# Performance work log

Hardware: AMD Instinct MI355X
Metric: run time of the kernel (lower is better)

The kernel has to match this reference:

```python
import jax, jax.numpy as jnp
import numpy as np
from jax.scipy.special import gammaln

# NQ_IN + 4 == 2*H is required because the two kernel=1, padding=1 convs grow the
# length axis by 4 and the following nn.Linear(2H, H) acts on the length axis.
B, NQ_IN, NK, QDIM, KDIM, H = 16, 2044, 1024, 80, 256, 1024


def setup_inputs() -> dict:
    ks = jax.random.split(jax.random.key(0), 14)
    s = 0.02
    return {
        "query": jax.random.normal(ks[0], (B, NQ_IN, QDIM), jnp.float32),
        "key": jax.random.normal(ks[1], (B, NK, KDIM), jnp.float32),
        "query_lens": jnp.full((B,), 2 * H, jnp.int32),
        "key_lens": jnp.full((B,), NK, jnp.int32),
        # query branch params (Conv1d k=1 stored as (out,in); Linear as (out,in))
        "qc1_w": jax.random.normal(ks[2], (2 * H, QDIM), jnp.float32) * s,
        "qc1_b": jax.random.normal(ks[3], (2 * H,), jnp.float32) * s,
        "qc2_w": jax.random.normal(ks[4], (2 * H, 2 * H), jnp.float32) * s,
        "qc2_b": jax.random.normal(ks[5], (2 * H,), jnp.float32) * s,
        "ql_w": jax.random.normal(ks[6], (H, 2 * H), jnp.float32) * s,
        "ql_b": jax.random.normal(ks[7], (H,), jnp.float32) * s,
        # key branch params
        "kc_w": jax.random.normal(ks[8], (H, KDIM, 3), jnp.float32) * s,
        "kc_b": jax.random.normal(ks[9], (H,), jnp.float32) * s,
        "kl1_w": jax.random.normal(ks[10], (2 * H, H), jnp.float32) * s,
        "kl1_b": jax.random.normal(ks[11], (2 * H,), jnp.float32) * s,
        "kl2_w": jax.random.normal(ks[12], (H, 2 * H), jnp.float32) * s,
        "kl2_b": jax.random.normal(ks[13], (H,), jnp.float32) * s,
    }


def _log_beta_binom(query_lens, key_lens, tq, tk):
    # Standard MAS beta-binomial alignment prior over a (tq, tk) grid.
    i = jnp.arange(tq, dtype=jnp.float32)[None, :, None]
    j = jnp.arange(tk, dtype=jnp.float32)[None, None, :]
    ql = query_lens.astype(jnp.float32)[:, None, None]
    kl = key_lens.astype(jnp.float32)[:, None, None]
    a = i + 1.0
    b = jnp.maximum(ql - i, 1.0)
    n = jnp.maximum(kl - 1.0, 0.0)
    nmj = jnp.maximum(n - j, 0.0)

    def betaln(x, y):
        return gammaln(x) + gammaln(y) - gammaln(x + y)

    logp = (gammaln(n + 1.0) - gammaln(j + 1.0) - gammaln(nmj + 1.0)
            + betaln(j + a, nmj + b) - betaln(a, b))
    valid = (i < ql) & (j < kl)
    return jnp.where(valid, logp, -1e9)


def _forward(query, key, query_lens, key_lens,
             qc1_w, qc1_b, qc2_w, qc2_b, ql_w, ql_b,
             kc_w, kc_b, kl1_w, kl1_b, kl2_w, kl2_b):
    # query branch: b n c -> b c n, two k=1/p=1 convs (pad length, pointwise), Linear over LENGTH axis
    q = jnp.transpose(query, (0, 2, 1))                       # (B, QDIM, NQ_IN)
    q = jnp.pad(q, ((0, 0), (0, 0), (1, 1)))
    q = jnp.einsum('bcn,oc->bon', q, qc1_w) + qc1_b[None, :, None]   # (B, 2H, NQ_IN+2)
    q = jnp.pad(q, ((0, 0), (0, 0), (1, 1)))
    q = jnp.einsum('bcn,oc->bon', q, qc2_w) + qc2_b[None, :, None]   # (B, 2H, 2H)
    q = jnp.einsum('bcn,hn->bch', q, ql_w) + ql_b                    # (B, 2H, H) Linear on length axis

    # key branch: b n c -> b c n, Conv1d k=3 p=1, then two Linears over LENGTH axis
    k = jnp.transpose(key, (0, 2, 1))                         # (B, KDIM, NK)
    k = jax.lax.conv_general_dilated(k, kc_w, (1,), ((1, 1),),
                                     dimension_numbers=('NCH', 'OIH', 'NCH'))
    k = k + kc_b[None, :, None]                               # (B, H, NK=H)
    k = jnp.einsum('bcn,on->bco', k, kl1_w) + kl1_b           # (B, H, 2H)
    k = jnp.einsum('bco,ho->bch', k, kl2_w) + kl2_b           # (B, H, H)

    # dist = -cdist(q, k), computed via the GEMM form (same as torch.cdist mm mode)
    sq = (jnp.sum(q * q, -1)[:, :, None] + jnp.sum(k * k, -1)[:, None, :]
          - 2.0 * jnp.einsum('bnd,bmd->bnm', q, k))           # (B, 2H, H)
    dist = -jnp.sqrt(jnp.maximum(sq, 1e-12))

    prior = _log_beta_binom(query_lens, key_lens, q.shape[1], k.shape[1])
    return jax.nn.log_softmax(dist + prior, axis=-1)


def reference(query, key, query_lens, key_lens,
              qc1_w, qc1_b, qc2_w, qc2_b, ql_w, ql_b,
              kc_w, kc_b, kl1_w, kl1_b, kl2_w, kl2_b):
    return _forward(query, key, query_lens, key_lens,
                    qc1_w, qc1_b, qc2_w, qc2_b, ql_w, ql_b,
                    kc_w, kc_b, kl1_w, kl1_b, kl2_w, kl2_b)
```

## Files before the change

### kernel.cpp

```cpp
#include <hip/hip_runtime.h>
#include <math.h>

typedef unsigned short u16;
typedef float floatx4 __attribute__((ext_vector_type(4)));
typedef __bf16 bf16x8 __attribute__((ext_vector_type(8)));

#define BB   16
#define TQ   2048
#define TK   1024
#define HH   1024
#define H2   2048
#define QD   80
#define QDP  128
#define KD   256
#define NQ   2044
#define NKEY 1024
#define T12N 3072

__device__ __forceinline__ u16 f2bf(float f) {
  unsigned int u = __float_as_uint(f);
  u = u + 0x7fffu + ((u >> 16) & 1u);
  return (u16)(u >> 16);
}
__device__ __forceinline__ float bf2f(u16 s) {
  return __uint_as_float(((unsigned int)s) << 16);
}
__device__ __forceinline__ float tgf(const float* __restrict__ tbl, int x) {
  return tbl[(x < 8191) ? (x < 0 ? 0 : x) : 8191];
}

__global__ __launch_bounds__(256) void prep_all_k(
    const float* __restrict__ qc2_w, const float* __restrict__ kl2_w,
    const float* __restrict__ ql_w, const float* __restrict__ kc_w,
    const float* __restrict__ kl1_w,
    u16* __restrict__ qc2w, u16* __restrict__ kl2w, u16* __restrict__ qlw2,
    u16* __restrict__ kcp, float* __restrict__ colsum1, float* __restrict__ tbl)
{
  long b = blockIdx.x;
  const int t = threadIdx.x;
  __shared__ float red[256];
  if (b < 16384) {
    long i = b * 256 + t; qc2w[i] = f2bf(qc2_w[i]); return;
  }
  b -= 16384;
  if (b < 8192) {
    long i = b * 256 + t; kl2w[i] = f2bf(kl2_w[i]); return;
  }
  b -= 8192;
  if (b < 8192) {
    long i = b * 256 + t;
    int n = (int)(i & 2047);
    int h = (int)(i >> 11);
    qlw2[i] = (n < NQ) ? f2bf(ql_w[(long)h * H2 + n + 2]) : (u16)0; return;
  }
  b -= 8192;
  if (b < 3072) {
    long i = b * 256 + t;
    int r = (int)(i % 768);
    int o = (int)(i / 768);
    int tt = r >> 8, d = r & 255;
    kcp[i] = f2bf(kc_w[((long)o * KD + d) * 3 + tt]); return;
  }
  b -= 3072;
  if (b < 2048) {
    const float* row = kl1_w + b * (long)HH;
    float s = row[t] + row[t + 256] + row[t + 512] + row[t + 768];
    red[t] = s; __syncthreads();
    for (int st = 128; st > 0; st >>= 1) { if (t < st) red[t] += red[t + st]; __syncthreads(); }
    if (!t) colsum1[b] = red[0];
    return;
  }
  b -= 2048;
  { int i = (int)(b * 256 + t); if (i < 8192) tbl[i] = i ? (float)lgamma((double)i) : 0.0f; }
}

__global__ __launch_bounds__(256) void tpack_k(
    const float* __restrict__ kl1_w, const float* __restrict__ qc1_w,
    const float* __restrict__ query,
    u16* __restrict__ kl1T, u16* __restrict__ qc1T, u16* __restrict__ qT)
{
  __shared__ float tile[64][65];
  int bid = blockIdx.x;
  const int tid = threadIdx.x;
  const int r4 = tid >> 6, c = tid & 63;
  const float* src; u16* dst;
  int sr0, sc0, srcR, srcC, srcStride, dstC;
  if (bid < 512) {
    sr0 = (bid >> 4) * 64; sc0 = (bid & 15) * 64;
    src = kl1_w; srcR = 2048; srcC = 1024; srcStride = 1024;
    dst = kl1T; dstC = 2048;
  } else if ((bid -= 512) < 64) {
    sr0 = (bid >> 1) * 64; sc0 = (bid & 1) * 64;
    src = qc1_w; srcR = 2048; srcC = QD; srcStride = QD;
    dst = qc1T; dstC = 2048;
  } else {
    bid -= 64;
    const int b16 = bid >> 6, r = bid & 63;
    sr0 = (r >> 1) * 64; sc0 = (r & 1) * 64;
    src = query + (long)b16 * NQ * QD; srcR = NQ; srcC = QD; srcStride = QD;
    dst = qT + (long)b16 * QDP * 2048; dstC = 2048;
  }
#pragma unroll
  for (int rr = r4; rr < 64; rr += 4) {
    const int gr = sr0 + rr, gc = sc0 + c;
    tile[rr][c] = (gr < srcR && gc < srcC) ? src[(long)gr * srcStride + gc] : 0.f;
  }
  __syncthreads();
#pragma unroll
  for (int rr = r4; rr < 64; rr += 4)
    dst[(long)(sc0 + rr) * dstC + sr0 + c] = f2bf(tile[c][rr]);
}

__global__ __launch_bounds__(256) void pack_kcolT_k(const float* __restrict__ key, u16* __restrict__ out) {
  __shared__ float tile[64][65];
  const int bid = blockIdx.x, tid = threadIdx.x;
  const int b = bid >> 6, r = bid & 63;
  const int m0 = (r >> 2) * 64;
  const int d0 = (r & 3) * 64;
  const int r4 = tid >> 6, c = tid & 63;
#pragma unroll
  for (int rr = r4; rr < 64; rr += 4)
    tile[rr][c] = key[((long)b * NKEY + m0 + rr) * KD + d0 + c];
  __syncthreads();
#pragma unroll
  for (int t = 0; t < 3; t++) {
    const int n = m0 + 1 - t + c;
    if (n >= 0 && n < NKEY) {
#pragma unroll
      for (int rr = r4; rr < 64; rr += 4)
        out[((long)b * 768 + t * 256 + d0 + rr) * NKEY + n] = f2bf(tile[c][rr]);
    }
  }
  if (m0 == 0 && c == 0) {
#pragma unroll
    for (int rr = r4; rr < 64; rr += 4)
      out[((long)b * 768 + d0 + rr) * NKEY + 0] = (u16)0;
  }
  if (m0 == 960 && c == 0) {
#pragma unroll
    for (int rr = r4; rr < 64; rr += 4)
      out[((long)b * 768 + 512 + d0 + rr) * NKEY + (NKEY - 1)] = (u16)0;
  }
}

__global__ __launch_bounds__(256) void fold_bias_k(
    const float* __restrict__ qc2_w, const float* __restrict__ qc1_b, const float* __restrict__ qc2_b,
    const float* __restrict__ kl2_w, const float* __restrict__ kl1_b, const float* __restrict__ kl2_b,
    const float* __restrict__ ql_w, const float* __restrict__ colsum1,
    float* __restrict__ bqm, float* __restrict__ bkv, float* __restrict__ s1v, float* __restrict__ s0v,
    float* __restrict__ wsum)
{
  const int bid = blockIdx.x, t = threadIdx.x;
  float s = 0.f, s2 = 0.f;
  if (bid < H2) {
    const float* row = qc2_w + (long)bid * H2;
    for (int k = t; k < H2; k += 256) s += row[k] * qc1_b[k];
  } else if (bid < H2 + HH) {
    const float* row = kl2_w + (long)(bid - H2) * H2;
    for (int k = t; k < H2; k += 256) { const float rv = row[k]; s += rv * kl1_b[k]; s2 += rv * colsum1[k]; }
  } else {
    const float* row = ql_w + (long)(bid - H2 - HH) * H2;
    for (int m = 1 + t; m <= H2 - 2; m += 256) s += row[m];
  }
  __shared__ float red[256];
  __shared__ float red2[256];
  red[t] = s; red2[t] = s2; __syncthreads();
  for (int st = 128; st > 0; st >>= 1) {
    if (t < st) { red[t] += red[t + st]; red2[t] += red2[t + st]; }
    __syncthreads();
  }
  if (!t) {
    if (bid < H2) bqm[bid] = red[0] + qc2_b[bid];
    else if (bid < H2 + HH) { bkv[bid - H2] = red[0] + kl2_b[bid - H2]; wsum[bid - H2] = red2[0]; }
    else {
      int h = bid - H2 - HH;
      s1v[h] = red[0];
      s0v[h] = ql_w[(long)h * H2] + ql_w[(long)h * H2 + H2 - 1];
    }
  }
}

__device__ __forceinline__ void gld_lds16(const u16* g, u16* l) {
  __builtin_amdgcn_global_load_lds((const __attribute__((address_space(1))) void*)g,
                                   (__attribute__((address_space(3))) void*)l, 16, 0, 0);
}

template<int OUTF32>
__global__ __launch_bounds__(256) void gemm_bt(
    const u16* __restrict__ A, const u16* __restrict__ B, void* __restrict__ Cv,
    int M, int N, int K, int lda, int ldb, int swap, int kspl,
    long sA, long sB, long sC, long sN,
    const float* __restrict__ colb, const float* __restrict__ rowb,
    const float* __restrict__ r1m, const float* __restrict__ r1n,
    const float* __restrict__ r2m, const float* __restrict__ r2n)
{
  __shared__ __align__(16) u16 As[128 * 32];
  __shared__ __align__(16) u16 Bs[128 * 32];
  const int bz = blockIdx.z;
  const int bb_ = (kspl > 1) ? bz / kspl : bz;
  const int ks_ = (kspl > 1) ? bz - bb_ * kspl : 0;
  const int tid  = threadIdx.x;
  const int lane = tid & 63;
  const int wv = tid >> 6;
  const int wm = ((tid >> 7) & 1) * 64;
  const int wn = ((tid >> 6) & 1) * 64;
  const int m0 = (swap ? blockIdx.x : blockIdx.y) * 128;
  const int n0 = (swap ? blockIdx.y : blockIdx.x) * 128;

  const int srow = wv * 32 + (lane >> 2);
  const int scol = (lane & 3) << 3;
  const u16* ga = A + bb_ * sA + (long)ks_ * K + (long)(m0 + srow) * lda + scol;
  const u16* gb = B + bb_ * sB + (long)ks_ * K + (long)(n0 + srow) * ldb + scol;
  u16* la0 = &As[(wv * 32) * 32];
  u16* la1 = &As[(wv * 32 + 16) * 32];
  u16* lb0 = &Bs[(wv * 32) * 32];
  u16* lb1 = &Bs[(wv * 32 + 16) * 32];
  const long a16 = (long)16 * lda;
  const long b16 = (long)16 * ldb;

  floatx4 acc[4][4];
#pragma unroll
  for (int a_ = 0; a_ < 4; a_++)
#pragma unroll
    for (int b_ = 0; b_ < 4; b_++) acc[a_][b_] = (floatx4){0.f, 0.f, 0.f, 0.f};

  const int fr = lane & 15;
  const int fk = (lane >> 4) << 3;

  for (int kb = 0; kb < K; kb += 32) {
    gld_lds16(ga,       la0);
    gld_lds16(ga + a16, la1);
    gld_lds16(gb,       lb0);
    gld_lds16(gb + b16, lb1);
    ga += 32; gb += 32;
    __syncthreads();
    bf16x8 af[4], bfr[4];
#pragma unroll
    for (int mi = 0; mi < 4; mi++)
      af[mi] = *reinterpret_cast<const bf16x8*>(&As[(wm + mi * 16 + fr) * 32 + fk]);
#pragma unroll
    for (int ni = 0; ni < 4; ni++)
      bfr[ni] = *reinterpret_cast<const bf16x8*>(&Bs[(wn + ni * 16 + fr) * 32 + fk]);
#pragma unroll
    for (int mi = 0; mi < 4; mi++)
#pragma unroll
      for (int ni = 0; ni < 4; ni++)
        acc[mi][ni] = __builtin_amdgcn_mfma_f32_16x16x32_bf16(af[mi], bfr[ni], acc[mi][ni], 0, 0, 0);
    __syncthreads();
  }

  const int fr4 = (lane >> 4) << 2;
  const int fc  = lane & 15;
  u16*   Cb16 = (u16*)Cv + (long)bz * sC;
  float* Cb32 = (float*)Cv + (long)bz * sC;
  const float* cbp  = colb ? colb + (long)bb_ * sN : nullptr;
  const float* r1np = r1n ? r1n + (long)bb_ * sN : nullptr;
  const float* r2np = r2n ? r2n + (long)bb_ * sN : nullptr;
#pragma unroll
  for (int mi = 0; mi < 4; mi++) {
#pragma unroll
    for (int ni = 0; ni < 4; ni++) {
      const int gm0 = m0 + wm + mi * 16 + fr4;
      const int gn  = n0 + wn + ni * 16 + fc;
      const float cbv  = cbp ? cbp[gn] : 0.f;
      const float r1nv = r1np ? r1np[gn] : 0.f;
      const float r2nv = r2np ? r2np[gn] : 0.f;
#pragma unroll
      for (int rr = 0; rr < 4; rr++) {
        const int gm = gm0 + rr;
        float v = acc[mi][ni][rr] + cbv;
        if (rowb) v += rowb[gm];
        if (r1m)  v += r1m[gm] * r1nv;
        if (r2m)  v += r2m[gm] * r2nv;
        if (OUTF32) Cb32[(long)gm * N + gn] = v;
        else        Cb16[(long)gm * N + gn] = f2bf(v);
      }
    }
  }
}

__global__ __launch_bounds__(256) void reduce_bk_k(const float* __restrict__ P, u16* __restrict__ out,
                                                   long chunk, int S, long total) {
  long j = ((long)blockIdx.x * 256 + threadIdx.x) * 4;
  if (j >= total) return;
  long b = j / chunk;
  const float* p = P + j + b * chunk * (S - 1);
  float4 s = *reinterpret_cast<const float4*>(p);
  for (int t = 1; t < S; t++) {
    const float4 v = *reinterpret_cast<const float4*>(p + (long)t * chunk);
    s.x += v.x; s.y += v.y; s.z += v.z; s.w += v.w;
  }
  union { u16 h[4]; uint2 u; } o;
  o.h[0] = f2bf(s.x); o.h[1] = f2bf(s.y); o.h[2] = f2bf(s.z); o.h[3] = f2bf(s.w);
  *reinterpret_cast<uint2*>(out + j) = o.u;
}

__global__ __launch_bounds__(256) void u_k(
    const u16* __restrict__ TpT, const float* __restrict__ qlb,
    const float* __restrict__ s1, const float* __restrict__ s0,
    const float* __restrict__ tbl, const int* __restrict__ qlens, const int* __restrict__ klens,
    float* __restrict__ u0, float* __restrict__ u1, float* __restrict__ u2,
    float* __restrict__ sc, float* __restrict__ c1,
    float* __restrict__ crow, float* __restrict__ t12)
{
  const int bid = blockIdx.x, t = threadIdx.x;
  __shared__ float4 red[256];
  if (bid < BB * QDP) {
    uint2 v = reinterpret_cast<const uint2*>(TpT + (long)bid * HH)[t];
    float a0 = bf2f((u16)(v.x & 0xffff)), a1 = bf2f((u16)(v.x >> 16));
    float a2 = bf2f((u16)(v.y & 0xffff)), a3 = bf2f((u16)(v.y >> 16));
    float4 q  = reinterpret_cast<const float4*>(qlb)[t];
    float4 w1 = reinterpret_cast<const float4*>(s1)[t];
    float4 w0 = reinterpret_cast<const float4*>(s0)[t];
    float4 s;
    s.x = a0 * q.x  + a1 * q.y  + a2 * q.z  + a3 * q.w;
    s.y = a0 * w1.x + a1 * w1.y + a2 * w1.z + a3 * w1.w;
    s.z = a0 * w0.x + a1 * w0.y + a2 * w0.z + a3 * w0.w;
    s.w = 0.f;
    red[t] = s; __syncthreads();
    for (int st = 128; st > 0; st >>= 1) {
      if (t < st) { red[t].x += red[t + st].x; red[t].y += red[t + st].y; red[t].z += red[t + st].z; }
      __syncthreads();
    }
    if (!t) { u0[bid] = red[0].x; u1[bid] = red[0].y; u2[bid] = red[0].z; }
  } else if (bid < BB * QDP + 6) {
    const int idx = bid - BB * QDP;
    const float* X = (idx == 1 || idx == 5) ? s1 : (idx == 2) ? s0 : qlb;
    const float* Y = (idx == 1 || idx == 3) ? s1 : (idx == 0) ? qlb : s0;
    float4 x = reinterpret_cast<const float4*>(X)[t];
    float4 y = reinterpret_cast<const float4*>(Y)[t];
    float4 s; s.x = x.x * y.x + x.y * y.y + x.z * y.z + x.w * y.w; s.y = s.z = s.w = 0.f;
    red[t] = s; __syncthreads();
    for (int st = 128; st > 0; st >>= 1) {
      if (t < st) red[t].x += red[t + st].x;
      __syncthreads();
    }
    if (!t) sc[idx] = red[0].x;
  } else if (bid < BB * QDP + 6 + 64) {
    const int idx = bid - (BB * QDP + 6);
    const int b = idx >> 2;
    const int j = ((idx & 3) << 8) | t;
    const int kl = klens[b];
    const int n_ = (kl - 1 > 0) ? kl - 1 : 0;
    c1[b * TK + j] = tgf(tbl, j + 1) + tgf(tbl, n_ - j + 1);
  } else if (bid < BB * QDP + 6 + 64 + 128) {
    const int idx = bid - (BB * QDP + 6 + 64);
    const int b = idx >> 3;
    const int i = ((idx & 7) << 8) | t;
    const int ql = qlens[b], kl = klens[b];
    const int n_ = (kl - 1 > 0) ? kl - 1 : 0;
    const int bb = (ql - i > 1) ? ql - i : 1;
    crow[b * TQ + i] = tgf(tbl, n_ + 1) + tgf(tbl, i + 1 + bb) - tgf(tbl, i + 1)
                     - tgf(tbl, bb) - tgf(tbl, i + 1 + n_ + bb);
  } else {
    const int idx = bid - (BB * QDP + 6 + 64 + 128);
    const int b = idx / 12;
    const int s = (idx - b * 12) * 256 + t;
    const int ql = qlens[b], kl = klens[b];
    const int n_ = (kl - 1 > 0) ? kl - 1 : 0;
    t12[b * T12N + s] = tgf(tbl, s + 1) + tgf(tbl, n_ + ql - s);
  }
}

__global__ __launch_bounds__(256) void qn_k(
    const u16* __restrict__ Wq, const float* __restrict__ WqG,
    const float* __restrict__ u0, const float* __restrict__ u1, const float* __restrict__ u2,
    const float* __restrict__ bqm, const float* __restrict__ qc2_b,
    const float* __restrict__ sc, float* __restrict__ qn)
{
  const int bx = blockIdx.x, t = threadIdx.x;
  const int b = bx >> 10;
  const int i = ((bx & 1023) << 1) | (t >> 7);
  const int d = t & 127;
  const float w  = bf2f(Wq[(long)i * QDP + d]);
  const float g  = WqG[((long)b * H2 + i) * QDP + d];
  const float bq = bqm[i], q2 = qc2_b[i];
  const float uu = u0[b * QDP + d] + bq * u1[b * QDP + d] + q2 * u2[b * QDP + d];
  __shared__ float red[256];
  red[t] = w * (g + 2.f * uu); __syncthreads();
  for (int s = 64; s > 0; s >>= 1) { if ((t & 127) < s) red[t] += red[t + s]; __syncthreads(); }
  if (d == 0) {
    const float cst = sc[0] + bq * bq * sc[1] + q2 * q2 * sc[2]
                    + 2.f * (bq * sc[3] + q2 * sc[4] + bq * q2 * sc[5]);
    qn[b * TQ + i] = red[t] + cst;
  }
}

__global__ __launch_bounds__(256) void rownormk_k(
    const u16* __restrict__ K3, const float* __restrict__ qlb,
    const float* __restrict__ s1, const float* __restrict__ s0,
    float* __restrict__ kn, float* __restrict__ yb, float* __restrict__ y1, float* __restrict__ y0)
{
  const long r = blockIdx.x;
  const int t = threadIdx.x;
  uint2 v = reinterpret_cast<const uint2*>(K3 + r * HH)[t];
  float a0 = bf2f((u16)(v.x & 0xffff)), a1 = bf2f((u16)(v.x >> 16));
  float a2 = bf2f((u16)(v.y & 0xffff)), a3 = bf2f((u16)(v.y >> 16));
  float4 q  = reinterpret_cast<const float4*>(qlb)[t];
  float4 w1 = reinterpret_cast<const float4*>(s1)[t];
  float4 w0 = reinterpret_cast<const float4*>(s0)[t];
  float4 s;
  s.x = a0 * a0   + a1 * a1   + a2 * a2   + a3 * a3;
  s.y = a0 * q.x  + a1 * q.y  + a2 * q.z  + a3 * q.w;
  s.z = a0 * w1.x + a1 * w1.y + a2 * w1.z + a3 * w1.w;
  s.w = a0 * w0.x + a1 * w0.y + a2 * w0.z + a3 * w0.w;
  __shared__ float4 red[256];
  red[t] = s; __syncthreads();
  for (int st = 128; st > 0; st >>= 1) {
    if (t < st) {
      red[t].x += red[t + st].x; red[t].y += red[t + st].y;
      red[t].z += red[t + st].z; red[t].w += red[t + st].w;
    }
    __syncthreads();
  }
  if (!t) { kn[r] = red[0].x; yb[r] = red[0].y; y1[r] = red[0].z; y0[r] = red[0].w; }
}

#define L2E 1.4426950408889634f
__global__ __launch_bounds__(1024) void smax_k(
    const u16* __restrict__ Wq, const u16* __restrict__ Z2, float* __restrict__ out,
    const float* __restrict__ ybv, const float* __restrict__ y1v, const float* __restrict__ y0v,
    const float* __restrict__ bqmv, const float* __restrict__ qc2_b,
    const float* __restrict__ qnv, const float* __restrict__ knv, const float* __restrict__ c1v,
    const float* __restrict__ crowv, const float* __restrict__ t12v,
    const int* __restrict__ qlens, const int* __restrict__ klens)
{
  __shared__ __align__(16) float wst[16][32 * 36];
  __shared__ float t12s[1152];
  __shared__ float jA[1024], jB[1024], jC[1024], jc1[1024];
  __shared__ float qns[128], crs[128], bqms[128], q2bs[128];
  __shared__ float lseb[4][128];
  __shared__ float lsef[128];

  const int b = blockIdx.x, mt = blockIdx.y;
  const int m0 = mt * 128;
  const int t = threadIdx.x;
  const int w = t >> 6, lane = t & 63;
  const int wm2 = (w >> 2) * 32;
  const int wn2 = (w & 3) * 32;
  const int fr = lane & 15, fk = (lane >> 4) << 3;
  const int fr4 = (lane >> 4) << 2, fc = lane & 15;
  const int qlv = qlens[b], klv = klens[b];

  if (t < 128) {
    qns[t]  = qnv[(long)b * TQ + m0 + t];
    crs[t]  = crowv[(long)b * TQ + m0 + t];
    bqms[t] = bqmv[m0 + t];
    q2bs[t] = qc2_b[m0 + t];
  }
  for (int k = t; k < 1152; k += 1024) t12s[k] = t12v[(long)b * T12N + m0 + k];
  {
    const int j = t;
    const float kn = knv[(long)b * TK + j];
    const float yb = ybv[(long)b * TK + j];
    const float y1 = y1v[(long)b * TK + j];
    const float y0 = y0v[(long)b * TK + j];
    jA[j]  = kn - 2.f * yb;
    jB[j]  = -2.f * y1;
    jC[j]  = -2.f * y0;
    jc1[j] = c1v[(long)b * TK + j];
  }

  bf16x8 af[4][2];
#pragma unroll
  for (int kc = 0; kc < 4; kc++)
#pragma unroll
    for (int mi = 0; mi < 2; mi++)
      af[kc][mi] = *reinterpret_cast<const bf16x8*>(
          Wq + (long)(m0 + wm2 + mi * 16 + fr) * QDP + kc * 32 + fk);

  const u16* Zb = Z2 + (long)b * TK * QDP;
  float* outp = out + (long)b * TQ * TK + (long)m0 * TK;

  float s_[8];
#pragma unroll
  for (int ri = 0; ri < 8; ri++) s_[ri] = 0.f;

  __syncthreads();

  for (int nt = 0; nt < 8; nt++) {
    bf16x8 bfr[4][2];
#pragma unroll
    for (int kc = 0; kc < 4; kc++)
#pragma unroll
      for (int nj = 0; nj < 2; nj++)
        bfr[kc][nj] = *reinterpret_cast<const bf16x8*>(
            Zb + (long)(nt * 128 + wn2 + nj * 16 + fr) * QDP + kc * 32 + fk);

    floatx4 acc[2][2];
#pragma unroll
    for (int mi = 0; mi < 2; mi++)
#pragma unroll
      for (int nj = 0; nj < 2; nj++) acc[mi][nj] = (floatx4){0.f, 0.f, 0.f, 0.f};
#pragma unroll
    for (int kc = 0; kc < 4; kc++)
#pragma unroll
      for (int mi = 0; mi < 2; mi++)
#pragma unroll
        for (int nj = 0; nj < 2; nj++)
          acc[mi][nj] = __builtin_amdgcn_mfma_f32_16x16x32_bf16(af[kc][mi], bfr[kc][nj], acc[mi][nj], 0, 0, 0);

    int gj[2]; float Aj[2], Bj[2], Cj[2], Dj[2];
#pragma unroll
    for (int nj = 0; nj < 2; nj++) {
      gj[nj] = nt * 128 + wn2 + nj * 16 + fc;
      Aj[nj] = jA[gj[nj]]; Bj[nj] = jB[gj[nj]]; Cj[nj] = jC[gj[nj]]; Dj[nj] = jc1[gj[nj]];
    }

#pragma unroll
    for (int mi = 0; mi < 2; mi++) {
#pragma unroll
      for (int rr = 0; rr < 4; rr++) {
        const int rl = wm2 + mi * 16 + fr4 + rr;
        const float qnr = qns[rl], crr = crs[rl], bqr = bqms[rl], q2r = q2bs[rl];
        const bool rowok = (m0 + rl) < qlv;
        const int ri = mi * 4 + rr;
#pragma unroll
        for (int nj = 0; nj < 2; nj++) {
          const float sq = fmaxf(qnr + Aj[nj] + bqr * Bj[nj] + q2r * Cj[nj]
                                 - 2.0f * acc[mi][nj][rr], 1e-12f);
          const float x = -__builtin_amdgcn_sqrtf(sq) + crr - Dj[nj] + t12s[rl + gj[nj]];
          const float vv = (rowok && gj[nj] < klv) ? x : -1e9f;
          s_[ri] += exp2f(vv * L2E);
        }
      }
    }
  }

#pragma unroll
  for (int k2 = 1; k2 <= 8; k2 <<= 1) {
#pragma unroll
    for (int ri = 0; ri < 8; ri++) s_[ri] += __shfl_xor(s_[ri], k2, 64);
  }
  if (fc == 0) {
#pragma unroll
    for (int mi = 0; mi < 2; mi++)
#pragma unroll
      for (int rr = 0; rr < 4; rr++)
        lseb[w & 3][wm2 + mi * 16 + fr4 + rr] = s_[mi * 4 + rr];
  }
  __syncthreads();
  if (t < 128) {
    const float tot = (lseb[0][t] + lseb[1][t]) + (lseb[2][t] + lseb[3][t]);
    lsef[t] = (tot > 0.f) ? logf(tot) : (-1e9f + logf((float)TK));
  }
  __syncthreads();

  float lse_r[8];
#pragma unroll
  for (int mi = 0; mi < 2; mi++)
#pragma unroll
    for (int rr = 0; rr < 4; rr++)
      lse_r[mi * 4 + rr] = lsef[wm2 + mi * 16 + fr4 + rr];

  float* wstw = wst[w];
  for (int nt = 0; nt < 8; nt++) {
    bf16x8 bfr[4][2];
#pragma unroll
    for (int kc = 0; kc < 4; kc++)
#pragma unroll
      for (int nj = 0; nj < 2; nj++)
        bfr[kc][nj] = *reinterpret_cast<const bf16x8*>(
            Zb + (long)(nt * 128 + wn2 + nj * 16 + fr) * QDP + kc * 32 + fk);

    floatx4 acc[2][2];
#pragma unroll
    for (int mi = 0; mi < 2; mi++)
#pragma unroll
      for (int nj = 0; nj < 2; nj++) acc[mi][nj] = (floatx4){0.f, 0.f, 0.f, 0.f};
#pragma unroll
    for (int kc = 0; kc < 4; kc++)
#pragma unroll
      for (int mi = 0; mi < 2; mi++)
#pragma unroll
        for (int nj = 0; nj < 2; nj++)
          acc[mi][nj] = __builtin_amdgcn_mfma_f32_16x16x32_bf16(af[kc][mi], bfr[kc][nj], acc[mi][nj], 0, 0, 0);

    int gj[2]; float Aj[2], Bj[2], Cj[2], Dj[2];
#pragma unroll
    for (int nj = 0; nj < 2; nj++) {
      gj[nj] = nt * 128 + wn2 + nj * 16 + fc;
      Aj[nj] = jA[gj[nj]]; Bj[nj] = jB[gj[nj]]; Cj[nj] = jC[gj[nj]]; Dj[nj] = jc1[gj[nj]];
    }

#pragma unroll
    for (int mi = 0; mi < 2; mi++) {
#pragma unroll
      for (int rr = 0; rr < 4; rr++) {
        const int rl = wm2 + mi * 16 + fr4 + rr;
        const float qnr = qns[rl], crr = crs[rl], bqr = bqms[rl], q2r = q2bs[rl];
        const bool rowok = (m0 + rl) < qlv;
        const float l = lse_r[mi * 4 + rr];
#pragma unroll
        for (int nj = 0; nj < 2; nj++) {
          const float sq = fmaxf(qnr + Aj[nj] + bqr * Bj[nj] + q2r * Cj[nj]
                                 - 2.0f * acc[mi][nj][rr], 1e-12f);
          const float x = -__builtin_amdgcn_sqrtf(sq) + crr - Dj[nj] + t12s[rl + gj[nj]];
          const float vv = (rowok && gj[nj] < klv) ? x : -1e9f;
          wstw[(mi * 16 + fr4 + rr) * 36 + nj * 16 + fc] = vv - l;
        }
      }
    }

#pragma unroll
    for (int st = 0; st < 4; st++) {
      const int lr2 = st * 8 + (lane >> 3);
      const int lc2 = (lane & 7) << 2;
      *reinterpret_cast<float4*>(outp + (long)(wm2 + lr2) * TK + nt * 128 + wn2 + lc2) =
          *reinterpret_cast<const float4*>(&wstw[lr2 * 36 + lc2]);
    }
  }
}

extern "C" void kernel_launch(void* const* d_in, const int* in_sizes, int n_in,
                              void* d_out, int out_size, void* d_ws, size_t ws_size,
                              hipStream_t stream)
{
  (void)in_sizes; (void)n_in; (void)out_size; (void)ws_size;
  const float* query = (const float*)d_in[0];
  const float* key   = (const float*)d_in[1];
  const int*   qlens = (const int*)d_in[2];
  const int*   klens = (const int*)d_in[3];
  const float* qc1_w = (const float*)d_in[4];
  const float* qc1_b = (const float*)d_in[5];
  const float* qc2_w = (const float*)d_in[6];
  const float* qc2_b = (const float*)d_in[7];
  const float* ql_w  = (const float*)d_in[8];
  const float* ql_b  = (const float*)d_in[9];
  const float* kc_w  = (const float*)d_in[10];
  const float* kc_b  = (const float*)d_in[11];
  const float* kl1_w = (const float*)d_in[12];
  const float* kl1_b = (const float*)d_in[13];
  const float* kl2_w = (const float*)d_in[14];
  const float* kl2_b = (const float*)d_in[15];

  size_t off = 0;
  char* ws = (char*)d_ws;
  auto alloc = [&](size_t bytes) -> char* {
    char* p = ws + off; off += (bytes + 255) & ~(size_t)255; return p;
  };
  u16* qc2w_bf = (u16*)alloc(2ull * H2 * H2);
  u16* qc1T_bf = (u16*)alloc(2ull * QDP * H2);
  u16* kl2w_bf = (u16*)alloc(2ull * HH * H2);
  u16* kl1T_bf = (u16*)alloc(2ull * HH * H2);
  u16* qT_bf   = (u16*)alloc(2ull * BB * QDP * 2048);
  u16* kcolT_bf= (u16*)d_ws;
  u16* Z2_bf   = (u16*)d_ws;
  u16* qlw2_bf = (u16*)alloc(2ull * HH * 2048);
  u16* kcp_bf  = (u16*)alloc(2ull * HH * 768);
  u16* TpT_bf  = (u16*)alloc(2ull * H2 * HH);
  char* pool   = alloc(2ull * BB * HH * NKEY);
  float* Pbuf  = (float*)pool;
  u16* X_bf    = (u16*)pool;
  float* tbl  = (float*)alloc(4ull * 8192);
  u16* Wq_bf  = (u16*)alloc(2ull * H2 * QDP);
  u16* Wk_bf  = (u16*)alloc(2ull * HH * NKEY);
  float* bqm  = (float*)alloc(4ull * H2);
  float* bkv  = (float*)alloc(4ull * HH);
  float* s1v  = (float*)alloc(4ull * HH);
  float* s0v  = (float*)alloc(4ull * HH);
  float* wsum = (float*)alloc(4ull * HH);
  float* colsum1 = (float*)alloc(4ull * H2);
  u16* K3_bf  = (u16*)alloc(2ull * BB * TK * HH);
  float* qnv  = (float*)alloc(4ull * BB * TQ);
  float* knv  = (float*)alloc(4ull * BB * TK);
  float* ybv  = (float*)alloc(4ull * BB * TK);
  float* y1v  = (float*)alloc(4ull * BB * TK);
  float* y0v  = (float*)alloc(4ull * BB * TK);
  float* u0v  = (float*)alloc(4ull * BB * QDP);
  float* u1v  = (float*)alloc(4ull * BB * QDP);
  float* u2v  = (float*)alloc(4ull * BB * QDP);
  float* c1v  = (float*)alloc(4ull * BB * TK);
  float* crowv= (float*)alloc(4ull * BB * TQ);
  float* t12v = (float*)alloc(4ull * BB * T12N);
  float* scv  = (float*)alloc(256);
  float* WqG  = (float*)d_out;
  u16* G_bf   = (u16*)((char*)d_out + 16777216);

  prep_all_k<<<37920, 256, 0, stream>>>(qc2_w, kl2_w, ql_w, kc_w, kl1_w,
                                        qc2w_bf, kl2w_bf, qlw2_bf, kcp_bf, colsum1, tbl);
  tpack_k<<<1600, 256, 0, stream>>>(kl1_w, qc1_w, query, kl1T_bf, qc1T_bf, qT_bf);
  fold_bias_k<<<4096, 256, 0, stream>>>(qc2_w, qc1_b, qc2_b, kl2_w, kl1_b, kl2_b, ql_w, colsum1,
                                        bqm, bkv, s1v, s0v, wsum);

  gemm_bt<1><<<dim3(1, 16, 16), 256, 0, stream>>>(qc2w_bf, qc1T_bf, Pbuf, H2, QDP, 128,
      H2, H2, 0, 16, 0, 0, (long)H2 * QDP, 0,
      nullptr, nullptr, nullptr, nullptr, nullptr, nullptr);
  reduce_bk_k<<<256, 256, 0, stream>>>(Pbuf, Wq_bf, (long)H2 * QDP, 16, (long)H2 * QDP);

  gemm_bt<1><<<dim3(8, 8, 8), 256, 0, stream>>>(kl2w_bf, kl1T_bf, Pbuf, HH, NKEY, 256,
      H2, H2, 0, 8, 0, 0, (long)HH * NKEY, 0,
      nullptr, nullptr, nullptr, nullptr, nullptr, nullptr);
  reduce_bk_k<<<1024, 256, 0, stream>>>(Pbuf, Wk_bf, (long)HH * NKEY, 8, (long)HH * NKEY);

  gemm_bt<1><<<dim3(8, 16, 4), 256, 0, stream>>>(qT_bf, qlw2_bf, Pbuf, H2, HH, 512,
      2048, 2048, 0, 4, 0, 0, (long)H2 * HH, 0,
      nullptr, nullptr, nullptr, nullptr, nullptr, nullptr);
  reduce_bk_k<<<2048, 256, 0, stream>>>(Pbuf, TpT_bf, (long)H2 * HH, 4, (long)H2 * HH);

  gemm_bt<1><<<dim3(1, 1, 128), 256, 0, stream>>>(TpT_bf, TpT_bf, Pbuf, 128, 128, 128,
      HH, HH, 0, 8, (long)QDP * HH, (long)QDP * HH, 128 * 128, 0,
      nullptr, nullptr, nullptr, nullptr, nullptr, nullptr);
  reduce_bk_k<<<256, 256, 0, stream>>>(Pbuf, G_bf, 128 * 128, 8, (long)BB * 128 * 128);

  gemm_bt<1><<<dim3(1, 16, 16), 256, 0, stream>>>(Wq_bf, G_bf, WqG, H2, QDP, QDP,
      QDP, QDP, 0, 1, 0, (long)QDP * QDP, (long)H2 * QDP, 0,
      nullptr, nullptr, nullptr, nullptr, nullptr, nullptr);
  u_k<<<BB * QDP + 6 + 64 + 128 + 192, 256, 0, stream>>>(TpT_bf, ql_b, s1v, s0v, tbl, qlens, klens,
                                                         u0v, u1v, u2v, scv, c1v, crowv, t12v);
  qn_k<<<BB * TQ / 2, 256, 0, stream>>>(Wq_bf, WqG, u0v, u1v, u2v, bqm, qc2_b, scv, qnv);

  pack_kcolT_k<<<1024, 256, 0, stream>>>(key, kcolT_bf);
  gemm_bt<0><<<dim3(6, 8, BB), 256, 0, stream>>>(Wk_bf, kcolT_bf, X_bf, HH, 768, NKEY,
      NKEY, NKEY, 0, 1, 0, (long)768 * NKEY, (long)HH * 768, 0,
      nullptr, nullptr, nullptr, nullptr, nullptr, nullptr);
  gemm_bt<0><<<dim3(8, 8, BB), 256, 0, stream>>>(kcp_bf, X_bf, K3_bf, HH, NKEY, 768,
      768, 768, 1, 1, 0, (long)HH * 768, (long)TK * HH, 0,
      bkv, nullptr, kc_b, wsum, nullptr, nullptr);

  gemm_bt<1><<<dim3(8, 1, 32), 256, 0, stream>>>(K3_bf, TpT_bf, Pbuf, TK, QDP, 512,
      HH, HH, 1, 2, (long)TK * HH, (long)QDP * HH, (long)TK * QDP, 0,
      nullptr, nullptr, nullptr, nullptr, nullptr, nullptr);
  reduce_bk_k<<<2048, 256, 0, stream>>>(Pbuf, Z2_bf, (long)TK * QDP, 2, (long)BB * TK * QDP);

  rownormk_k<<<BB * TK, 256, 0, stream>>>(K3_bf, ql_b, s1v, s0v, knv, ybv, y1v, y0v);

  smax_k<<<dim3(16, 16), 1024, 0, stream>>>(Wq_bf, Z2_bf, (float*)d_out,
      ybv, y1v, y0v, bqm, qc2_b, qnv, knv, c1v, crowv, t12v, qlens, klens);
}
```

Baseline: 611.9 us.

## Shrink softmax tile to 32 rows, drop LDS staging, raise occupancy

The fused distance/log-softmax kernel now handles 32 query rows per block with 512 threads instead of 128 rows with 1024 threads, and launches four times as many blocks. The 72 KB per-block output staging buffer is removed, and results are written straight from MFMA accumulator layout to global memory. Per-row constants and the log-sum-exp offset are hoisted into registers. The aim is more resident waves and less LDS pressure, at the cost of narrower, less coalesced stores and reloading the shared per-batch column vectors in many more blocks.

After: 726.9 us. +18.8%, slower.

```diff
diff --git a/kernel.cpp b/kernel.cpp
--- a/kernel.cpp
+++ b/kernel.cpp
@@ -417,7 +417,7 @@
 }
 
 #define L2E 1.4426950408889634f
-__global__ __launch_bounds__(1024) void smax_k(
+__global__ __launch_bounds__(512, 8) void smax_k(
     const u16* __restrict__ Wq, const u16* __restrict__ Z2, float* __restrict__ out,
     const float* __restrict__ ybv, const float* __restrict__ y1v, const float* __restrict__ y0v,
     const float* __restrict__ bqmv, const float* __restrict__ qc2_b,
@@ -425,58 +425,64 @@
     const float* __restrict__ crowv, const float* __restrict__ t12v,
     const int* __restrict__ qlens, const int* __restrict__ klens)
 {
-  __shared__ __align__(16) float wst[16][32 * 36];
-  __shared__ float t12s[1152];
+  __shared__ float t12s[1056];
   __shared__ float jA[1024], jB[1024], jC[1024], jc1[1024];
-  __shared__ float qns[128], crs[128], bqms[128], q2bs[128];
-  __shared__ float lseb[4][128];
-  __shared__ float lsef[128];
+  __shared__ float qns[32], crs[32], bqms[32], q2bs[32];
+  __shared__ float lseb[4][32];
+  __shared__ float lsef[32];
 
   const int b = blockIdx.x, mt = blockIdx.y;
-  const int m0 = mt * 128;
+  const int m0 = mt * 32;
   const int t = threadIdx.x;
   const int w = t >> 6, lane = t & 63;
-  const int wm2 = (w >> 2) * 32;
+  const int wm2 = (w >> 2) * 16;
   const int wn2 = (w & 3) * 32;
   const int fr = lane & 15, fk = (lane >> 4) << 3;
   const int fr4 = (lane >> 4) << 2, fc = lane & 15;
   const int qlv = qlens[b], klv = klens[b];
 
-  if (t < 128) {
+  if (t < 32) {
     qns[t]  = qnv[(long)b * TQ + m0 + t];
     crs[t]  = crowv[(long)b * TQ + m0 + t];
     bqms[t] = bqmv[m0 + t];
     q2bs[t] = qc2_b[m0 + t];
   }
-  for (int k = t; k < 1152; k += 1024) t12s[k] = t12v[(long)b * T12N + m0 + k];
-  {
-    const int j = t;
-    const float kn = knv[(long)b * TK + j];
-    const float yb = ybv[(long)b * TK + j];
-    const float y1 = y1v[(long)b * TK + j];
-    const float y0 = y0v[(long)b * TK + j];
-    jA[j]  = kn - 2.f * yb;
-    jB[j]  = -2.f * y1;
-    jC[j]  = -2.f * y0;
-    jc1[j] = c1v[(long)b * TK + j];
-  }
-
-  bf16x8 af[4][2];
+  for (int k = t; k < 1056; k += 512) t12s[k] = t12v[(long)b * T12N + m0 + k];
+#pragma unroll
+  for (int k = t; k < 1024; k += 512) {
+    const float kn = knv[(long)b * TK + k];
+    const float yb = ybv[(long)b * TK + k];
+    const float y1 = y1v[(long)b * TK + k];
+    const float y0 = y0v[(long)b * TK + k];
+    jA[k]  = kn - 2.f * yb;
+    jB[k]  = -2.f * y1;
+    jC[k]  = -2.f * y0;
+    jc1[k] = c1v[(long)b * TK + k];
+  }
+
+  bf16x8 af[4];
 #pragma unroll
   for (int kc = 0; kc < 4; kc++)
-#pragma unroll
-    for (int mi = 0; mi < 2; mi++)
-      af[kc][mi] = *reinterpret_cast<const bf16x8*>(
-          Wq + (long)(m0 + wm2 + mi * 16 + fr) * QDP + kc * 32 + fk);
+    af[kc] = *reinterpret_cast<const bf16x8*>(
+        Wq + (long)(m0 + wm2 + fr) * QDP + kc * 32 + fk);
 
   const u16* Zb = Z2 + (long)b * TK * QDP;
   float* outp = out + (long)b * TQ * TK + (long)m0 * TK;
 
-  float s_[8];
-#pragma unroll
-  for (int ri = 0; ri < 8; ri++) s_[ri] = 0.f;
-
   __syncthreads();
+
+  float qnr[4], crr[4], bqr4[4], q2r4[4];
+  bool rowok[4];
+#pragma unroll
+  for (int rr = 0; rr < 4; rr++) {
+    const int rl = wm2 + fr4 + rr;
+    qnr[rr] = qns[rl]; crr[rr] = crs[rl]; bqr4[rr] = bqms[rl]; q2r4[rr] = q2bs[rl];
+    rowok[rr] = (m0 + rl) < qlv;
+  }
+
+  float s_[4];
+#pragma unroll
+  for (int rr = 0; rr < 4; rr++) s_[rr] = 0.f;
 
   for (int nt = 0; nt < 8; nt++) {
     bf16x8 bfr[4][2];
@@ -487,42 +493,33 @@
         bfr[kc][nj] = *reinterpret_cast<const bf16x8*>(
             Zb + (long)(nt * 128 + wn2 + nj * 16 + fr) * QDP + kc * 32 + fk);
 
-    floatx4 acc[2][2];
-#pragma unroll
-    for (int mi = 0; mi < 2; mi++)
-#pragma unroll
-      for (int nj = 0; nj < 2; nj++) acc[mi][nj] = (floatx4){0.f, 0.f, 0.f, 0.f};
+    floatx4 acc[2];
+#pragma unroll
+    for (int nj = 0; nj < 2; nj++) acc[nj] = (floatx4){0.f, 0.f, 0.f, 0.f};
 #pragma unroll
     for (int kc = 0; kc < 4; kc++)
 #pragma unroll
-      for (int mi = 0; mi < 2; mi++)
-#pragma unroll
-        for (int nj = 0; nj < 2; nj++)
-          acc[mi][nj] = __builtin_amdgcn_mfma_f32_16x16x32_bf16(af[kc][mi], bfr[kc][nj], acc[mi][nj], 0, 0, 0);
-
-    int gj[2]; float Aj[2], Bj[2], Cj[2], Dj[2];
+      for (int nj = 0; nj < 2; nj++)
+        acc[nj] = __builtin_amdgcn_mfma_f32_16x16x32_bf16(af[kc], bfr[kc][nj], acc[nj], 0, 0, 0);
+
+    int gj[2]; float Aj[2], Bj[2], Cj[2], Dj[2]; bool colok[2];
 #pragma unroll
     for (int nj = 0; nj < 2; nj++) {
       gj[nj] = nt * 128 + wn2 + nj * 16 + fc;
       Aj[nj] = jA[gj[nj]]; Bj[nj] = jB[gj[nj]]; Cj[nj] = jC[gj[nj]]; Dj[nj] = jc1[gj[nj]];
-    }
-
-#pragma unroll
-    for (int mi = 0; mi < 2; mi++) {
-#pragma unroll
-      for (int rr = 0; rr < 4; rr++) {
-        const int rl = wm2 + mi * 16 + fr4 + rr;
-        const float qnr = qns[rl], crr = crs[rl], bqr = bqms[rl], q2r = q2bs[rl];
-        const bool rowok = (m0 + rl) < qlv;
-        const int ri = mi * 4 + rr;
-#pragma unroll
-        for (int nj = 0; nj < 2; nj++) {
-          const float sq = fmaxf(qnr + Aj[nj] + bqr * Bj[nj] + q2r * Cj[nj]
-                                 - 2.0f * acc[mi][nj][rr], 1e-12f);
-          const float x = -__builtin_amdgcn_sqrtf(sq) + crr - Dj[nj] + t12s[rl + gj[nj]];
-          const float vv = (rowok && gj[nj] < klv) ? x : -1e9f;
-          s_[ri] += exp2f(vv * L2E);
-        }
+      colok[nj] = gj[nj] < klv;
+    }
+
+#pragma unroll
+    for (int rr = 0; rr < 4; rr++) {
+      const int rl = wm2 + fr4 + rr;
+#pragma unroll
+      for (int nj = 0; nj < 2; nj++) {
+        const float sq = fmaxf(qnr[rr] + Aj[nj] + bqr4[rr] * Bj[nj] + q2r4[rr] * Cj[nj]
+                               - 2.0f * acc[nj][rr], 1e-12f);
+        const float x = -__builtin_amdgcn_sqrtf(sq) + crr[rr] - Dj[nj] + t12s[rl + gj[nj]];
+        const float vv = (rowok[rr] && colok[nj]) ? x : -1e9f;
+        s_[rr] += exp2f(vv * L2E);
       }
     }
   }
@@ -530,30 +527,28 @@
 #pragma unroll
   for (int k2 = 1; k2 <= 8; k2 <<= 1) {
 #pragma unroll
-    for (int ri = 0; ri < 8; ri++) s_[ri] += __shfl_xor(s_[ri], k2, 64);
+    for (int rr = 0; rr < 4; rr++) s_[rr] += __shfl_xor(s_[rr], k2, 64);
   }
   if (fc == 0) {
 #pragma unroll
-    for (int mi = 0; mi < 2; mi++)
-#pragma unroll
-      for (int rr = 0; rr < 4; rr++)
-        lseb[w & 3][wm2 + mi * 16 + fr4 + rr] = s_[mi * 4 + rr];
+    for (int rr = 0; rr < 4; rr++)
+      lseb[w & 3][wm2 + fr4 + rr] = s_[rr];
   }
   __syncthreads();
-  if (t < 128) {
+  if (t < 32) {
     const float tot = (lseb[0][t] + lseb[1][t]) + (lseb[2][t] + lseb[3][t]);
     lsef[t] = (tot > 0.f) ? logf(tot) : (-1e9f + logf((float)TK));
   }
   __syncthreads();
 
-  float lse_r[8];
-#pragma unroll
-  for (int mi = 0; mi < 2; mi++)
-#pragma unroll
-    for (int rr = 0; rr < 4; rr++)
-      lse_r[mi * 4 + rr] = lsef[wm2 + mi * 16 + fr4 + rr];
-
-  float* wstw = wst[w];
+  float crl[4], mneg[4];
+#pragma unroll
+  for (int rr = 0; rr < 4; rr++) {
+    const float l = lsef[wm2 + fr4 + rr];
+    crl[rr]  = crr[rr] - l;
+    mneg[rr] = -1e9f - l;
+  }
+
   for (int nt = 0; nt < 8; nt++) {
     bf16x8 bfr[4][2];
 #pragma unroll
@@ -563,51 +558,34 @@
         bfr[kc][nj] = *reinterpret_cast<const bf16x8*>(
             Zb + (long)(nt * 128 + wn2 + nj * 16 + fr) * QDP + kc * 32 + fk);
 
-    floatx4 acc[2][2];
-#pragma unroll
-    for (int mi = 0; mi < 2; mi++)
-#pragma unroll
-      for (int nj = 0; nj < 2; nj++) acc[mi][nj] = (floatx4){0.f, 0.f, 0.f, 0.f};
+    floatx4 acc[2];
+#pragma unroll
+    for (int nj = 0; nj < 2; nj++) acc[nj] = (floatx4){0.f, 0.f, 0.f, 0.f};
 #pragma unroll
     for (int kc = 0; kc < 4; kc++)
 #pragma unroll
-      for (int mi = 0; mi < 2; mi++)
-#pragma unroll
-        for (int nj = 0; nj < 2; nj++)
-          acc[mi][nj] = __builtin_amdgcn_mfma_f32_16x16x32_bf16(af[kc][mi], bfr[kc][nj], acc[mi][nj], 0, 0, 0);
-
-    int gj[2]; float Aj[2], Bj[2], Cj[2], Dj[2];
+      for (int nj = 0; nj < 2; nj++)
+        acc[nj] = __builtin_amdgcn_mfma_f32_16x16x32_bf16(af[kc], bfr[kc][nj], acc[nj], 0, 0, 0);
+
+    int gj[2]; float Aj[2], Bj[2], Cj[2], Dj[2]; bool colok[2];
 #pragma unroll
     for (int nj = 0; nj < 2; nj++) {
       gj[nj] = nt * 128 + wn2 + nj * 16 + fc;
       Aj[nj] = jA[gj[nj]]; Bj[nj] = jB[gj[nj]]; Cj[nj] = jC[gj[nj]]; Dj[nj] = jc1[gj[nj]];
-    }
-
-#pragma unroll
-    for (int mi = 0; mi < 2; mi++) {
-#pragma unroll
-      for (int rr = 0; rr < 4; rr++) {
-        const int rl = wm2 + mi * 16 + fr4 + rr;
-        const float qnr = qns[rl], crr = crs[rl], bqr = bqms[rl], q2r = q2bs[rl];
-        const bool rowok = (m0 + rl) < qlv;
-        const float l = lse_r[mi * 4 + rr];
-#pragma unroll
-        for (int nj = 0; nj < 2; nj++) {
-          const float sq = fmaxf(qnr + Aj[nj] + bqr * Bj[nj] + q2r * Cj[nj]
-                                 - 2.0f * acc[mi][nj][rr], 1e-12f);
-          const float x = -__builtin_amdgcn_sqrtf(sq) + crr - Dj[nj] + t12s[rl + gj[nj]];
-          const float vv = (rowok && gj[nj] < klv) ? x : -1e9f;
-          wstw[(mi * 16 + fr4 + rr) * 36 + nj * 16 + fc] = vv - l;
-        }
+      colok[nj] = gj[nj] < klv;
+    }
+
+#pragma unroll
+    for (int rr = 0; rr < 4; rr++) {
+      const int rl = wm2 + fr4 + rr;
+#pragma unroll
+      for (int nj = 0; nj < 2; nj++) {
+        const float sq = fmaxf(qnr[rr] + Aj[nj] + bqr4[rr] * Bj[nj] + q2r4[rr] * Cj[nj]
+                               - 2.0f * acc[nj][rr], 1e-12f);
+        const float x = -__builtin_amdgcn_sqrtf(sq) + crl[rr] - Dj[nj] + t12s[rl + gj[nj]];
+        const float res = (rowok[rr] && colok[nj]) ? x : mneg[rr];
+        outp[(long)rl * TK + gj[nj]] = res;
       }
-    }
-
-#pragma unroll
-    for (int st = 0; st < 4; st++) {
-      const int lr2 = st * 8 + (lane >> 3);
-      const int lc2 = (lane & 7) << 2;
-      *reinterpret_cast<float4*>(outp + (long)(wm2 + lr2) * TK + nt * 128 + wn2 + lc2) =
-          *reinterpret_cast<const float4*>(&wstw[lr2 * 36 + lc2]);
     }
   }
 }
@@ -725,6 +703,6 @@
 
   rownormk_k<<<BB * TK, 256, 0, stream>>>(K3_bf, ql_b, s1v, s0v, knv, ybv, y1v, y0v);
 
-  smax_k<<<dim3(16, 16), 1024, 0, stream>>>(Wq_bf, Z2_bf, (float*)d_out,
+  smax_k<<<dim3(16, 64), 512, 0, stream>>>(Wq_bf, Z2_bf, (float*)d_out,
       ybv, y1v, y0v, bqm, qc2_b, qnv, knv, c1v, crowv, t12v, qlens, klens);
 }
```
